# Kernel tuning notes

Hardware: AMD Instinct MI355X
Metric: run time of the kernel (lower is better)

## Reference

```python
import jax, jax.numpy as jnp
import numpy as np

U_NUM = 100000
I_NUM = 50000
D = 64
L = 3
N_EDGES = 1000000
N_SEDGES = 500000


def setup_inputs() -> dict:
    key = jax.random.key(0)
    k1, k2, k3, k4, k5, k6, k7 = jax.random.split(key, 7)
    return {
        "user_emb": jax.random.normal(k1, (U_NUM, D), dtype=jnp.float32),
        "item_emb": jax.random.normal(k2, (I_NUM, D), dtype=jnp.float32),
        "edge_user": jax.random.randint(k3, (N_EDGES,), 0, U_NUM, dtype=jnp.int32),
        "edge_item": jax.random.randint(k4, (N_EDGES,), 0, I_NUM, dtype=jnp.int32),
        "s_row": jax.random.randint(k5, (N_SEDGES,), 0, I_NUM, dtype=jnp.int32),
        "s_col": jax.random.randint(k6, (N_SEDGES,), 0, I_NUM, dtype=jnp.int32),
        "s_val": jax.random.uniform(k7, (N_SEDGES,), dtype=jnp.float32),
    }


def reference(user_emb, item_emb, edge_user, edge_item, s_row, s_col, s_val):
    U = user_emb.shape[0]
    I = item_emb.shape[0]
    M = U + I  # size of joint user-item graph

    # symmetric bipartite adjacency edge list (items offset by U)
    r = jnp.concatenate([edge_user, edge_item + U])
    c = jnp.concatenate([edge_item + U, edge_user])
    ones = jnp.ones(r.shape[0], dtype=user_emb.dtype)

    # D^{-1/2} (A) D^{-1/2} normalization with +1 smoothing, as in _create_adjacency_matrix
    deg_row = jax.ops.segment_sum(ones, r, num_segments=M)
    deg_col = jax.ops.segment_sum(ones, c, num_segments=M)
    norm_r = jax.lax.rsqrt(deg_row + 1.0)
    norm_c = jax.lax.rsqrt(deg_col + 1.0)
    vals = norm_r[r] * norm_c[c]  # [2E]

    # s_hat enhanced item-item edges (indices offset by U as in _s_hat_sparse)
    sr = s_row + U
    sc = s_col + U

    cur = jnp.concatenate([user_emb, item_emb], axis=0)  # [M, D]
    acc = cur
    for _ in range(L):
        msg = jax.ops.segment_sum(vals[:, None] * cur[c], r, num_segments=M)
        enh = jax.ops.segment_sum(s_val[:, None] * cur[sc], sr, num_segments=M)
        cur = msg + enh
        acc = acc + cur
    return acc / (L + 1)  # mean over all L+1 layer embeddings
```

## Files before the change

kernel.cpp:

```cpp
#include <hip/hip_runtime.h>

#define EMB_D 64
#define CSHIFT 9
#define CROWS  (1 << CSHIFT)
#define CMASK  (CROWS - 1)
#define MAXC 384
#define CPAD 16
#define SFLAG (1 << 27)
#define EPB 4096

typedef float    float4v __attribute__((ext_vector_type(4)));
typedef _Float16 half4v  __attribute__((ext_vector_type(4)));

__device__ inline float4v tof32(half4v v)  { return __builtin_convertvector(v, float4v); }

__global__ void __launch_bounds__(256) class_cnt(const int* __restrict__ eu,
                                                 const int* __restrict__ ei,
                                                 int E, int nbE,
                                                 const int* __restrict__ sr, int S,
                                                 int U, int* __restrict__ ctot) {
    __shared__ int hist[MAXC];
    for (int t = threadIdx.x; t < MAXC; t += 256) hist[t] = 0;
    __syncthreads();
    int blk = blockIdx.x;
    if (blk < nbE) {
        int e0 = blk * EPB, e1 = min(e0 + EPB, E);
        for (int e = e0 + threadIdx.x; e < e1; e += 256) {
            atomicAdd(&hist[eu[e] >> CSHIFT], 1);
            atomicAdd(&hist[(U + ei[e]) >> CSHIFT], 1);
        }
    } else {
        int e0 = (blk - nbE) * EPB, e1 = min(e0 + EPB, S);
        for (int e = e0 + threadIdx.x; e < e1; e += 256) {
            atomicAdd(&hist[(U + sr[e]) >> CSHIFT], 1);
        }
    }
    __syncthreads();
    for (int t = threadIdx.x; t < MAXC; t += 256) {
        int h = hist[t];
        if (h) atomicAdd(&ctot[t * CPAD], h);
    }
}

__global__ void __launch_bounds__(512) class_scan(int* __restrict__ ctot, int NC,
                                                  int* __restrict__ bkptr) {
    __shared__ int sh[512];
    int t = threadIdx.x;
    int v = (t < NC) ? ctot[t * CPAD] : 0;
    sh[t] = v;
    __syncthreads();
    for (int ofs = 1; ofs < 512; ofs <<= 1) {
        int x = (t >= ofs) ? sh[t - ofs] : 0;
        __syncthreads();
        sh[t] += x;
        __syncthreads();
    }
    int excl = sh[t] - v;
    if (t < NC) {
        bkptr[t] = excl;
        ctot[t * CPAD] = excl;
    }
    if (t == 511) bkptr[NC] = sh[511];
}

__global__ void __launch_bounds__(256) bin_kernel(const int* __restrict__ eu,
                                                  const int* __restrict__ ei,
                                                  int E, int nbE,
                                                  const int* __restrict__ sr,
                                                  const int* __restrict__ sc,
                                                  const float* __restrict__ sv, int S,
                                                  int U,
                                                  int* __restrict__ bkcur,
                                                  int2* __restrict__ bent) {
    __shared__ int hist[MAXC];
    __shared__ int base[MAXC];
    for (int t = threadIdx.x; t < MAXC; t += 256) hist[t] = 0;
    __syncthreads();

    int blk = blockIdx.x;
    if (blk < nbE) {
        int e0 = blk * EPB, e1 = min(e0 + EPB, E);
        for (int e = e0 + threadIdx.x; e < e1; e += 256) {
            atomicAdd(&hist[eu[e] >> CSHIFT], 1);
            atomicAdd(&hist[(U + ei[e]) >> CSHIFT], 1);
        }
        __syncthreads();
        for (int t = threadIdx.x; t < MAXC; t += 256) {
            int h = hist[t];
            base[t] = h ? atomicAdd(&bkcur[t * CPAD], h) : 0;
            hist[t] = 0;
        }
        __syncthreads();
        for (int e = e0 + threadIdx.x; e < e1; e += 256) {
            int u  = eu[e];
            int iv = U + ei[e];
            int c0 = u >> CSHIFT, c1 = iv >> CSHIFT;
            int o0 = atomicAdd(&hist[c0], 1);
            bent[base[c0] + o0] = make_int2(((u & CMASK) << 18) | iv, 0);
            int o1 = atomicAdd(&hist[c1], 1);
            bent[base[c1] + o1] = make_int2(((iv & CMASK) << 18) | u, 0);
        }
    } else {
        int e0 = (blk - nbE) * EPB, e1 = min(e0 + EPB, S);
        for (int e = e0 + threadIdx.x; e < e1; e += 256) {
            atomicAdd(&hist[(U + sr[e]) >> CSHIFT], 1);
        }
        __syncthreads();
        for (int t = threadIdx.x; t < MAXC; t += 256) {
            int h = hist[t];
            base[t] = h ? atomicAdd(&bkcur[t * CPAD], h) : 0;
            hist[t] = 0;
        }
        __syncthreads();
        for (int e = e0 + threadIdx.x; e < e1; e += 256) {
            int dst = U + sr[e];
            int c = dst >> CSHIFT;
            int o = atomicAdd(&hist[c], 1);
            bent[base[c] + o] = make_int2(SFLAG | ((dst & CMASK) << 18) | (U + sc[e]),
                                          __float_as_int(sv[e]));
        }
    }
}

__global__ void __launch_bounds__(1024) scatter_cls(const int* __restrict__ bkptr,
                                                    const int2* __restrict__ bent,
                                                    float* __restrict__ norm,
                                                    int* __restrict__ rowptr,
                                                    int2* __restrict__ ent, int M) {
    __shared__ int cntb[CROWS];
    __shared__ int cntt[CROWS];
    __shared__ int cur[CROWS];
    int c   = blockIdx.x;
    int rlo = c << CSHIFT;
    int nrows = min(CROWS, M - rlo);
    if (threadIdx.x < CROWS) {
        cntb[threadIdx.x] = 0;
        cntt[threadIdx.x] = 0;
    }
    __syncthreads();

    int beg = bkptr[c], end = bkptr[c + 1];
    for (int k = beg + threadIdx.x; k < end; k += 1024) {
        int x = bent[k].x;
        int rl = (x >> 18) & CMASK;
        atomicAdd(&cntt[rl], 1);
        if (!(x & SFLAG)) atomicAdd(&cntb[rl], 1);
    }
    __syncthreads();

    int my = 0;
    if (threadIdx.x < CROWS) {
        my = cntt[threadIdx.x];
        if (threadIdx.x < nrows)
            norm[rlo + threadIdx.x] = rsqrtf((float)cntb[threadIdx.x] + 1.0f);
    }
    for (int ofs = 1; ofs < CROWS; ofs <<= 1) {
        int x = (threadIdx.x >= ofs && threadIdx.x < CROWS) ? cntt[threadIdx.x - ofs] : 0;
        __syncthreads();
        if (threadIdx.x < CROWS) cntt[threadIdx.x] += x;
        __syncthreads();
    }
    if (threadIdx.x < CROWS) {
        int v = beg + cntt[threadIdx.x] - my;
        if (threadIdx.x < nrows) rowptr[rlo + threadIdx.x] = v;
        cur[threadIdx.x] = v;
    }
    if (threadIdx.x == 0) rowptr[rlo + nrows] = end;
    __syncthreads();

    for (int k = beg + threadIdx.x; k < end; k += 1024) {
        int2 e = bent[k];
        int rl  = (e.x >> 18) & CMASK;
        int col = e.x & 0x3FFFF;
        int p = atomicAdd(&cur[rl], 1);
        ent[p] = (e.x & SFLAG) ? make_int2(col, e.y)
                               : make_int2(col, (rlo + rl) | (int)0x80000000);
    }
}

__global__ void __launch_bounds__(256) fill_w(const float* __restrict__ norm,
                                              int2* __restrict__ ent, int NT) {
    int k = blockIdx.x * 256 + threadIdx.x;
    if (k >= NT) return;
    int2 e = ent[k];
    if (e.y < 0) {
        int row = e.y & 0x7FFFFFFF;
        e.y = __float_as_int(norm[row] * norm[e.x]);
        ent[k] = e;
    }
}

__global__ void init_kernel(const float4v* __restrict__ ue, const float4v* __restrict__ ie,
                            long u4, long total4, half4v* __restrict__ curH) {
    long stride = (long)gridDim.x * blockDim.x;
    for (long idx = (long)blockIdx.x * blockDim.x + threadIdx.x; idx < total4; idx += stride) {
        float4v v = (idx < u4) ? ue[idx] : ie[idx - u4];
        curH[idx] = __builtin_convertvector(v, half4v);
    }
}

template <int MODE>
__global__ void __launch_bounds__(256) gather_kernel(const int* __restrict__ rowptr,
                                                     const int2* __restrict__ ent,
                                                     const _Float16* __restrict__ curH,
                                                     const _Float16* __restrict__ cur0H,
                                                     _Float16* __restrict__ dstH,
                                                     float* __restrict__ out,
                                                     int U, int I, int M) {
    int raw = (int)((((long)blockIdx.x * blockDim.x) + threadIdx.x) >> 4);
    int l   = threadIdx.x & 15;
    if (raw >= M) return;
    int row = (raw < I) ? (U + raw) : (raw - I);
    int beg = rowptr[row];
    int end = rowptr[row + 1];
    const half4v* curv = (const half4v*)(const void*)curH;

    float4v acc = {0.f, 0.f, 0.f, 0.f};
    int j = beg;
    int2 a0 = (j + 0 < end) ? ent[j + 0] : make_int2(0, 0);
    int2 a1 = (j + 1 < end) ? ent[j + 1] : make_int2(0, 0);
    int2 a2 = (j + 2 < end) ? ent[j + 2] : make_int2(0, 0);
    int2 a3 = (j + 3 < end) ? ent[j + 3] : make_int2(0, 0);
    half4v v0 = curv[(long)a0.x * 16 + l];
    half4v v1 = curv[(long)a1.x * 16 + l];
    half4v v2 = curv[(long)a2.x * 16 + l];
    half4v v3 = curv[(long)a3.x * 16 + l];
    while (j + 4 < end) {
        int jn = j + 4;
        int2 b0 = (jn + 0 < end) ? ent[jn + 0] : make_int2(0, 0);
        int2 b1 = (jn + 1 < end) ? ent[jn + 1] : make_int2(0, 0);
        int2 b2 = (jn + 2 < end) ? ent[jn + 2] : make_int2(0, 0);
        int2 b3 = (jn + 3 < end) ? ent[jn + 3] : make_int2(0, 0);
        half4v u0 = curv[(long)b0.x * 16 + l];
        half4v u1 = curv[(long)b1.x * 16 + l];
        half4v u2 = curv[(long)b2.x * 16 + l];
        half4v u3 = curv[(long)b3.x * 16 + l];
        acc += __int_as_float(a0.y) * tof32(v0);
        acc += __int_as_float(a1.y) * tof32(v1);
        acc += __int_as_float(a2.y) * tof32(v2);
        acc += __int_as_float(a3.y) * tof32(v3);
        a0 = b0; a1 = b1; a2 = b2; a3 = b3;
        v0 = u0; v1 = u1; v2 = u2; v3 = u3;
        j = jn;
    }
    acc += __int_as_float(a0.y) * tof32(v0);
    acc += __int_as_float(a1.y) * tof32(v1);
    acc += __int_as_float(a2.y) * tof32(v2);
    acc += __int_as_float(a3.y) * tof32(v3);

    long o4 = (long)row * 16 + l;
    if (MODE == 0) {
        ((half4v*)dstH)[o4] = __builtin_convertvector(acc, half4v);
    } else if (MODE == 1) {
        float4v e0 = tof32(((const half4v*)cur0H)[o4]);
        float4v e1 = tof32(curv[o4]);
        ((half4v*)dstH)[o4] = __builtin_convertvector(acc, half4v);
        ((float4v*)out)[o4] = e0 + e1 + acc;
    } else {
        float4v pv = ((const float4v*)out)[o4];
        ((float4v*)out)[o4] = 0.25f * (pv + acc);
    }
}

extern "C" void kernel_launch(void* const* d_in, const int* in_sizes, int n_in,
                              void* d_out, int out_size, void* d_ws, size_t ws_size,
                              hipStream_t stream) {
    const float* user_emb = (const float*)d_in[0];
    const float* item_emb = (const float*)d_in[1];
    const int*   edge_user = (const int*)d_in[2];
    const int*   edge_item = (const int*)d_in[3];
    const int*   s_row = (const int*)d_in[4];
    const int*   s_col = (const int*)d_in[5];
    const float* s_val = (const float*)d_in[6];
    float* out = (float*)d_out;

    const int U = in_sizes[0] / EMB_D;
    const int I = in_sizes[1] / EMB_D;
    const int M = U + I;
    const int E = in_sizes[2];
    const int S = in_sizes[4];
    const long MD = (long)M * EMB_D;
    const long NT = 2L * E + S;
    const int NC = (M + CMASK) >> CSHIFT;

    char* p = (char*)d_ws;
    auto carve = [&](long bytes) {
        char* q = p;
        p += (bytes + 15) & ~15L;
        return q;
    };
    _Float16* cur0H = (_Float16*)carve(MD * sizeof(_Float16));
    _Float16* cur1H = (_Float16*)carve(MD * sizeof(_Float16));
    long aliasBytes = MD * (long)sizeof(_Float16) > (NT + 8) * (long)sizeof(int2)
                        ? MD * (long)sizeof(_Float16) : (NT + 8) * (long)sizeof(int2);
    char* aliasRgn = carve(aliasBytes);
    _Float16* cur2H = (_Float16*)aliasRgn;
    int2*     bent  = (int2*)aliasRgn;
    float* norm   = (float*)carve((long)M * sizeof(float));
    int*   rowptr = (int*)carve((long)(M + 1) * sizeof(int));
    int*   ctot   = (int*)carve((long)MAXC * CPAD * sizeof(int));
    int*   bkptr  = (int*)carve((long)(MAXC + 1) * sizeof(int));
    int2*  ent    = (int2*)carve((NT + 8) * sizeof(int2));

    const int nbE2 = (E + EPB - 1) / EPB;
    const int nbS2 = (S + EPB - 1) / EPB;

    hipMemsetAsync(ctot, 0, (size_t)MAXC * CPAD * sizeof(int), stream);
    class_cnt<<<nbE2 + nbS2, 256, 0, stream>>>(edge_user, edge_item, E, nbE2,
                                               s_row, S, U, ctot);

    class_scan<<<1, 512, 0, stream>>>(ctot, NC, bkptr);

    bin_kernel<<<nbE2 + nbS2, 256, 0, stream>>>(edge_user, edge_item, E, nbE2,
                                                s_row, s_col, s_val, S,
                                                U, ctot, bent);

    scatter_cls<<<NC, 1024, 0, stream>>>(bkptr, bent, norm, rowptr, ent, M);

    fill_w<<<(int)((NT + 255) / 256), 256, 0, stream>>>(norm, ent, (int)NT);

    init_kernel<<<2048, 256, 0, stream>>>((const float4v*)user_emb, (const float4v*)item_emb,
                                          (long)U * (EMB_D / 4), MD / 4, (half4v*)cur0H);

    const int gblocks = (int)(((long)M * 16 + 255) / 256);
    gather_kernel<0><<<gblocks, 256, 0, stream>>>(rowptr, ent, cur0H, nullptr,
                                                  cur1H, nullptr, U, I, M);
    gather_kernel<1><<<gblocks, 256, 0, stream>>>(rowptr, ent, cur1H, cur0H,
                                                  cur2H, out, U, I, M);
    gather_kernel<2><<<gblocks, 256, 0, stream>>>(rowptr, ent, cur2H, nullptr,
                                                  nullptr, out, U, I, M);
}
```

Before: 274.7 us.

## Precompute per-block class offsets and widen gather to 8-half vectors

The binning pass now stores per-block class histograms and runs a column-wise exclusive scan, so bin_kernel reads its offsets directly instead of recounting its edges and doing global atomics. This drops the memset and one histogram pass over the edge arrays, at the cost of an extra small scan kernel. Separately, the gather kernels move from 16 lanes with 4-half loads per row to 8 lanes with 8-half (16-byte) loads. That halves the thread count per row and widens each memory access, but raises register use per thread.

Result: faster. 240.8 us (-12.3%).

```diff
diff --git a/kernel.cpp b/kernel.cpp
--- a/kernel.cpp
+++ b/kernel.cpp
@@ -5,20 +5,21 @@
 #define CROWS  (1 << CSHIFT)
 #define CMASK  (CROWS - 1)
 #define MAXC 384
-#define CPAD 16
 #define SFLAG (1 << 27)
 #define EPB 4096
 
 typedef float    float4v __attribute__((ext_vector_type(4)));
+typedef float    float8v __attribute__((ext_vector_type(8)));
 typedef _Float16 half4v  __attribute__((ext_vector_type(4)));
-
-__device__ inline float4v tof32(half4v v)  { return __builtin_convertvector(v, float4v); }
+typedef _Float16 half8v  __attribute__((ext_vector_type(8)));
+
+__device__ inline float8v tof32x8(half8v v) { return __builtin_convertvector(v, float8v); }
 
 __global__ void __launch_bounds__(256) class_cnt(const int* __restrict__ eu,
                                                  const int* __restrict__ ei,
                                                  int E, int nbE,
                                                  const int* __restrict__ sr, int S,
-                                                 int U, int* __restrict__ ctot) {
+                                                 int U, int* __restrict__ percls) {
     __shared__ int hist[MAXC];
     for (int t = threadIdx.x; t < MAXC; t += 256) hist[t] = 0;
     __syncthreads();
@@ -36,17 +37,33 @@
         }
     }
     __syncthreads();
-    for (int t = threadIdx.x; t < MAXC; t += 256) {
-        int h = hist[t];
-        if (h) atomicAdd(&ctot[t * CPAD], h);
-    }
-}
-
-__global__ void __launch_bounds__(512) class_scan(int* __restrict__ ctot, int NC,
+    for (int t = threadIdx.x; t < MAXC; t += 256)
+        percls[(long)blk * MAXC + t] = hist[t];
+}
+
+__global__ void __launch_bounds__(512) colscan(int* __restrict__ percls, int NB,
+                                               int* __restrict__ ctot) {
+    __shared__ int sh[512];
+    int c = blockIdx.x;
+    int t = threadIdx.x;
+    int v = (t < NB) ? percls[(long)t * MAXC + c] : 0;
+    sh[t] = v;
+    __syncthreads();
+    for (int ofs = 1; ofs < 512; ofs <<= 1) {
+        int x = (t >= ofs) ? sh[t - ofs] : 0;
+        __syncthreads();
+        sh[t] += x;
+        __syncthreads();
+    }
+    if (t < NB) percls[(long)t * MAXC + c] = sh[t] - v;
+    if (t == 511) ctot[c] = sh[511];
+}
+
+__global__ void __launch_bounds__(512) class_scan(const int* __restrict__ ctot, int NC,
                                                   int* __restrict__ bkptr) {
     __shared__ int sh[512];
     int t = threadIdx.x;
-    int v = (t < NC) ? ctot[t * CPAD] : 0;
+    int v = (t < NC) ? ctot[t] : 0;
     sh[t] = v;
     __syncthreads();
     for (int ofs = 1; ofs < 512; ofs <<= 1) {
@@ -55,11 +72,7 @@
         sh[t] += x;
         __syncthreads();
     }
-    int excl = sh[t] - v;
-    if (t < NC) {
-        bkptr[t] = excl;
-        ctot[t * CPAD] = excl;
-    }
+    if (t < NC) bkptr[t] = sh[t] - v;
     if (t == 511) bkptr[NC] = sh[511];
 }
 
@@ -70,27 +83,20 @@
                                                   const int* __restrict__ sc,
                                                   const float* __restrict__ sv, int S,
                                                   int U,
-                                                  int* __restrict__ bkcur,
+                                                  const int* __restrict__ bkptr,
+                                                  const int* __restrict__ percls,
                                                   int2* __restrict__ bent) {
     __shared__ int hist[MAXC];
     __shared__ int base[MAXC];
-    for (int t = threadIdx.x; t < MAXC; t += 256) hist[t] = 0;
-    __syncthreads();
-
     int blk = blockIdx.x;
+    for (int t = threadIdx.x; t < MAXC; t += 256) {
+        base[t] = bkptr[t] + percls[(long)blk * MAXC + t];
+        hist[t] = 0;
+    }
+    __syncthreads();
+
     if (blk < nbE) {
         int e0 = blk * EPB, e1 = min(e0 + EPB, E);
-        for (int e = e0 + threadIdx.x; e < e1; e += 256) {
-            atomicAdd(&hist[eu[e] >> CSHIFT], 1);
-            atomicAdd(&hist[(U + ei[e]) >> CSHIFT], 1);
-        }
-        __syncthreads();
-        for (int t = threadIdx.x; t < MAXC; t += 256) {
-            int h = hist[t];
-            base[t] = h ? atomicAdd(&bkcur[t * CPAD], h) : 0;
-            hist[t] = 0;
-        }
-        __syncthreads();
         for (int e = e0 + threadIdx.x; e < e1; e += 256) {
             int u  = eu[e];
             int iv = U + ei[e];
@@ -102,16 +108,6 @@
         }
     } else {
         int e0 = (blk - nbE) * EPB, e1 = min(e0 + EPB, S);
-        for (int e = e0 + threadIdx.x; e < e1; e += 256) {
-            atomicAdd(&hist[(U + sr[e]) >> CSHIFT], 1);
-        }
-        __syncthreads();
-        for (int t = threadIdx.x; t < MAXC; t += 256) {
-            int h = hist[t];
-            base[t] = h ? atomicAdd(&bkcur[t * CPAD], h) : 0;
-            hist[t] = 0;
-        }
-        __syncthreads();
         for (int e = e0 + threadIdx.x; e < e1; e += 256) {
             int dst = U + sr[e];
             int c = dst >> CSHIFT;
@@ -207,58 +203,58 @@
                                                      _Float16* __restrict__ dstH,
                                                      float* __restrict__ out,
                                                      int U, int I, int M) {
-    int raw = (int)((((long)blockIdx.x * blockDim.x) + threadIdx.x) >> 4);
-    int l   = threadIdx.x & 15;
+    int raw = (int)((((long)blockIdx.x * blockDim.x) + threadIdx.x) >> 3);
+    int l   = threadIdx.x & 7;
     if (raw >= M) return;
     int row = (raw < I) ? (U + raw) : (raw - I);
     int beg = rowptr[row];
     int end = rowptr[row + 1];
-    const half4v* curv = (const half4v*)(const void*)curH;
-
-    float4v acc = {0.f, 0.f, 0.f, 0.f};
+    const half8v* curv = (const half8v*)(const void*)curH;
+
+    float8v acc = {0.f, 0.f, 0.f, 0.f, 0.f, 0.f, 0.f, 0.f};
     int j = beg;
     int2 a0 = (j + 0 < end) ? ent[j + 0] : make_int2(0, 0);
     int2 a1 = (j + 1 < end) ? ent[j + 1] : make_int2(0, 0);
     int2 a2 = (j + 2 < end) ? ent[j + 2] : make_int2(0, 0);
     int2 a3 = (j + 3 < end) ? ent[j + 3] : make_int2(0, 0);
-    half4v v0 = curv[(long)a0.x * 16 + l];
-    half4v v1 = curv[(long)a1.x * 16 + l];
-    half4v v2 = curv[(long)a2.x * 16 + l];
-    half4v v3 = curv[(long)a3.x * 16 + l];
+    half8v v0 = curv[(long)a0.x * 8 + l];
+    half8v v1 = curv[(long)a1.x * 8 + l];
+    half8v v2 = curv[(long)a2.x * 8 + l];
+    half8v v3 = curv[(long)a3.x * 8 + l];
     while (j + 4 < end) {
         int jn = j + 4;
         int2 b0 = (jn + 0 < end) ? ent[jn + 0] : make_int2(0, 0);
         int2 b1 = (jn + 1 < end) ? ent[jn + 1] : make_int2(0, 0);
         int2 b2 = (jn + 2 < end) ? ent[jn + 2] : make_int2(0, 0);
         int2 b3 = (jn + 3 < end) ? ent[jn + 3] : make_int2(0, 0);
-        half4v u0 = curv[(long)b0.x * 16 + l];
-        half4v u1 = curv[(long)b1.x * 16 + l];
-        half4v u2 = curv[(long)b2.x * 16 + l];
-        half4v u3 = curv[(long)b3.x * 16 + l];
-        acc += __int_as_float(a0.y) * tof32(v0);
-        acc += __int_as_float(a1.y) * tof32(v1);
-        acc += __int_as_float(a2.y) * tof32(v2);
-        acc += __int_as_float(a3.y) * tof32(v3);
+        half8v u0 = curv[(long)b0.x * 8 + l];
+        half8v u1 = curv[(long)b1.x * 8 + l];
+        half8v u2 = curv[(long)b2.x * 8 + l];
+        half8v u3 = curv[(long)b3.x * 8 + l];
+        acc += __int_as_float(a0.y) * tof32x8(v0);
+        acc += __int_as_float(a1.y) * tof32x8(v1);
+        acc += __int_as_float(a2.y) * tof32x8(v2);
+        acc += __int_as_float(a3.y) * tof32x8(v3);
         a0 = b0; a1 = b1; a2 = b2; a3 = b3;
         v0 = u0; v1 = u1; v2 = u2; v3 = u3;
         j = jn;
     }
-    acc += __int_as_float(a0.y) * tof32(v0);
-    acc += __int_as_float(a1.y) * tof32(v1);
-    acc += __int_as_float(a2.y) * tof32(v2);
-    acc += __int_as_float(a3.y) * tof32(v3);
-
-    long o4 = (long)row * 16 + l;
+    acc += __int_as_float(a0.y) * tof32x8(v0);
+    acc += __int_as_float(a1.y) * tof32x8(v1);
+    acc += __int_as_float(a2.y) * tof32x8(v2);
+    acc += __int_as_float(a3.y) * tof32x8(v3);
+
+    long o8 = (long)row * 8 + l;
     if (MODE == 0) {
-        ((half4v*)dstH)[o4] = __builtin_convertvector(acc, half4v);
+        ((half8v*)dstH)[o8] = __builtin_convertvector(acc, half8v);
     } else if (MODE == 1) {
-        float4v e0 = tof32(((const half4v*)cur0H)[o4]);
-        float4v e1 = tof32(curv[o4]);
-        ((half4v*)dstH)[o4] = __builtin_convertvector(acc, half4v);
-        ((float4v*)out)[o4] = e0 + e1 + acc;
+        float8v e0 = tof32x8(((const half8v*)cur0H)[o8]);
+        float8v e1 = tof32x8(curv[o8]);
+        ((half8v*)dstH)[o8] = __builtin_convertvector(acc, half8v);
+        ((float8v*)out)[o8] = e0 + e1 + acc;
     } else {
-        float4v pv = ((const float4v*)out)[o4];
-        ((float4v*)out)[o4] = 0.25f * (pv + acc);
+        float8v pv = ((const float8v*)out)[o8];
+        ((float8v*)out)[o8] = 0.25f * (pv + acc);
     }
 }
 
@@ -282,6 +278,10 @@
     const long MD = (long)M * EMB_D;
     const long NT = 2L * E + S;
     const int NC = (M + CMASK) >> CSHIFT;
+
+    const int nbE2 = (E + EPB - 1) / EPB;
+    const int nbS2 = (S + EPB - 1) / EPB;
+    const int NB = nbE2 + nbS2;
 
     char* p = (char*)d_ws;
     auto carve = [&](long bytes) {
@@ -298,22 +298,20 @@
     int2*     bent  = (int2*)aliasRgn;
     float* norm   = (float*)carve((long)M * sizeof(float));
     int*   rowptr = (int*)carve((long)(M + 1) * sizeof(int));
-    int*   ctot   = (int*)carve((long)MAXC * CPAD * sizeof(int));
+    int*   percls = (int*)carve((long)NB * MAXC * sizeof(int));
+    int*   ctot   = (int*)carve((long)MAXC * sizeof(int));
     int*   bkptr  = (int*)carve((long)(MAXC + 1) * sizeof(int));
     int2*  ent    = (int2*)carve((NT + 8) * sizeof(int2));
 
-    const int nbE2 = (E + EPB - 1) / EPB;
-    const int nbS2 = (S + EPB - 1) / EPB;
-
-    hipMemsetAsync(ctot, 0, (size_t)MAXC * CPAD * sizeof(int), stream);
-    class_cnt<<<nbE2 + nbS2, 256, 0, stream>>>(edge_user, edge_item, E, nbE2,
-                                               s_row, S, U, ctot);
-
+    class_cnt<<<NB, 256, 0, stream>>>(edge_user, edge_item, E, nbE2,
+                                      s_row, S, U, percls);
+
+    colscan<<<NC, 512, 0, stream>>>(percls, NB, ctot);
     class_scan<<<1, 512, 0, stream>>>(ctot, NC, bkptr);
 
-    bin_kernel<<<nbE2 + nbS2, 256, 0, stream>>>(edge_user, edge_item, E, nbE2,
-                                                s_row, s_col, s_val, S,
-                                                U, ctot, bent);
+    bin_kernel<<<NB, 256, 0, stream>>>(edge_user, edge_item, E, nbE2,
+                                       s_row, s_col, s_val, S,
+                                       U, bkptr, percls, bent);
 
     scatter_cls<<<NC, 1024, 0, stream>>>(bkptr, bent, norm, rowptr, ent, M);
 
@@ -322,7 +320,7 @@
     init_kernel<<<2048, 256, 0, stream>>>((const float4v*)user_emb, (const float4v*)item_emb,
                                           (long)U * (EMB_D / 4), MD / 4, (half4v*)cur0H);
 
-    const int gblocks = (int)(((long)M * 16 + 255) / 256);
+    const int gblocks = (int)(((long)M * 8 + 255) / 256);
     gather_kernel<0><<<gblocks, 256, 0, stream>>>(rowptr, ent, cur0H, nullptr,
                                                   cur1H, nullptr, U, I, M);
     gather_kernel<1><<<gblocks, 256, 0, stream>>>(rowptr, ent, cur1H, cur0H,
```
